# Kernel tuning notes

Hardware: AMD Instinct MI355X
Metric: run time of the kernel (lower is better)

The kernel has to match this reference:

```python
import jax, jax.numpy as jnp
import numpy as np

B, M, K, C = 256, 512, 6, 32  # graphs, nodes/graph, knn k, channels
IN_DIM, OUT_DIM = 4, 6


def setup_inputs() -> dict:
    key = jax.random.key(0)
    ks = jax.random.split(key, 20)
    N = B * M
    x = jax.random.normal(ks[0], (N, 1), dtype=jnp.float32)
    pos = jax.random.uniform(ks[1], (N, 3), dtype=jnp.float32)
    batch = jnp.repeat(jnp.arange(B, dtype=jnp.int64), M)

    def lin(k, out_d, in_d):
        bound = 1.0 / np.sqrt(in_d)
        kw, kb = jax.random.split(k)
        W = jax.random.uniform(kw, (out_d, in_d), minval=-bound, maxval=bound, dtype=jnp.float32)
        b = jax.random.uniform(kb, (out_d,), minval=-bound, maxval=bound, dtype=jnp.float32)
        return W, b

    W1a, b1a = lin(ks[2], C, IN_DIM)
    W2a, b2a = lin(ks[3], C, C)
    W1b, b1b = lin(ks[4], C, C)
    W2b, b2b = lin(ks[5], C, C)
    W1c, b1c = lin(ks[6], C, C)
    W2c, b2c = lin(ks[7], C, C)
    Wr, br = lin(ks[8], OUT_DIM, C)
    return dict(x=x, pos=pos, batch=batch,
                W1a=W1a, b1a=b1a, W2a=W2a, b2a=b2a,
                W1b=W1b, b1b=b1b, W2b=W2b, b2b=b2b,
                W1c=W1c, b1c=b1c, W2c=W2c, b2c=b2c,
                Wr=Wr, br=br)


def knn_indices(pos3):
    # pos3: [B, M, 3] -> [B, M, K] indices of K nearest neighbors (self included, loop=True)
    sq = jnp.sum(pos3 * pos3, axis=-1)                      # [B, M]
    d2 = sq[:, :, None] + sq[:, None, :] - 2.0 * jnp.einsum('bmd,bnd->bmn', pos3, pos3)
    _, idx = jax.lax.top_k(-d2, K)                          # [B, M, K]
    return idx


def gcn_layer(h, idx, W1, b1, W2, b2):
    # h: [B, M, Cin]; gather h_j per edge, 2-layer MLP per edge, max-aggregate over neighbors
    Cin = h.shape[-1]
    nb = jnp.take_along_axis(h, idx.reshape(B, M * K, 1), axis=1).reshape(B, M, K, Cin)
    msg = jax.nn.relu(jnp.einsum('bmkc,oc->bmko', nb, W1) + b1)
    msg = jnp.einsum('bmkc,oc->bmko', msg, W2) + b2
    return jnp.max(msg, axis=2)                             # max aggregation -> [B, M, C]


def reference(x, pos, batch,
              W1a, b1a, W2a, b2a,
              W1b, b1b, W2b, b2b,
              W1c, b1c, W2c, b2c,
              Wr, br):
    pos3 = pos.reshape(B, M, 3)
    idx = knn_indices(pos3)
    h = jnp.concatenate([x, pos], axis=-1).reshape(B, M, IN_DIM)
    h = jax.nn.relu(gcn_layer(h, idx, W1a, b1a, W2a, b2a))
    h = jax.nn.relu(gcn_layer(h, idx, W1b, b1b, W2b, b2b))
    h = jax.nn.relu(gcn_layer(h, idx, W1c, b1c, W2c, b2c))
    g = jnp.max(h, axis=1)                                  # global_max_pool -> [B, C]
    return g @ Wr.T + br                                    # [B, 6]
```

## Files before the change

### kernel.cpp

```cpp
#include <hip/hip_runtime.h>
#include <cstddef>

#define NB 256
#define M 512
#define KNN 6
#define C 32

__global__ __launch_bounds__(1024, 1) void megafused_kernel(
    const float* __restrict__ x, const float* __restrict__ pos,
    const float* __restrict__ W1a, const float* __restrict__ b1a,
    const float* __restrict__ W2a, const float* __restrict__ b2a,
    const float* __restrict__ W1b, const float* __restrict__ b1b,
    const float* __restrict__ W2b, const float* __restrict__ b2b,
    const float* __restrict__ W1c, const float* __restrict__ b1c,
    const float* __restrict__ W2c, const float* __restrict__ b2c,
    const float* __restrict__ Wr,  const float* __restrict__ br,
    float* __restrict__ out)
{
    __shared__ __align__(16) float Ts[M * C];
    const int g  = blockIdx.x;
    const int t  = threadIdx.x;
    const int n  = t & (M - 1);
    const int hv = t >> 9;
    const int c0 = __builtin_amdgcn_readfirstlane(hv << 4);

    float4* sp          = (float4*)Ts;
    float*  cd          = Ts + 2048;
    unsigned short* ci  = (unsigned short*)(Ts + 2048 + 7168);

    const float* p = pos + (size_t)g * M * 3;
    if (t < M) {
        float xx = p[3*t], yy = p[3*t+1], zz = p[3*t+2];
        sp[t] = make_float4(xx, yy, zz, fmaf(xx, xx, fmaf(yy, yy, zz * zz)));
    }
    __syncthreads();

    const float4 pm = sp[n];

    float d0 = INFINITY, d1 = INFINITY, d2 = INFINITY,
          d3 = INFINITY, d4 = INFINITY, d5 = INFINITY;
    int   i0 = -1, i1 = -1, i2 = -1, i3 = -1, i4 = -1, i5 = -1;

    const int col0 = hv << 8;
#pragma unroll 4
    for (int jj = 0; jj < 256; jj++) {
        const int col = col0 + jj;
        const float4 pn = sp[col];
        float dot  = fmaf(pm.x, pn.x, fmaf(pm.y, pn.y, pm.z * pn.z));
        float dist = fmaf(-2.f, dot, pm.w + pn.w);
        bool c5 = dist < d5, c4 = dist < d4, c3 = dist < d3,
             c2 = dist < d2, c1 = dist < d1, cz = dist < d0;
        i5 = c4 ? i4 : (c5 ? col : i5);
        i4 = c3 ? i3 : (c4 ? col : i4);
        i3 = c2 ? i2 : (c3 ? col : i3);
        i2 = c1 ? i1 : (c2 ? col : i2);
        i1 = cz ? i0 : (c1 ? col : i1);
        i0 = cz ? col : i0;
        d5 = __builtin_amdgcn_fmed3f(dist, d4, d5);
        d4 = __builtin_amdgcn_fmed3f(dist, d3, d4);
        d3 = __builtin_amdgcn_fmed3f(dist, d2, d3);
        d2 = __builtin_amdgcn_fmed3f(dist, d1, d2);
        d1 = __builtin_amdgcn_fmed3f(dist, d0, d1);
        d0 = fminf(dist, d0);
    }
    {
        float* cdp = cd + t * 7;
        cdp[0]=d0; cdp[1]=d1; cdp[2]=d2; cdp[3]=d3; cdp[4]=d4; cdp[5]=d5;
        unsigned short* cip = ci + t * 7;
        cip[0]=(unsigned short)i0; cip[1]=(unsigned short)i1;
        cip[2]=(unsigned short)i2; cip[3]=(unsigned short)i3;
        cip[4]=(unsigned short)i4; cip[5]=(unsigned short)i5;
    }
    __syncthreads();

    int j[KNN];
    {
        float md[KNN]; int mi[KNN];
#pragma unroll
        for (int k = 0; k < KNN; k++) { md[k] = cd[n*7 + k]; mi[k] = ci[n*7 + k]; }
        const int L1 = (n + M) * 7;
#pragma unroll
        for (int k = 0; k < KNN; k++) {
            float dist = cd[L1 + k];
            int   nn   = ci[L1 + k];
            bool c5 = dist < md[5], c4 = dist < md[4], c3 = dist < md[3],
                 c2 = dist < md[2], c1 = dist < md[1], cz = dist < md[0];
            mi[5] = c4 ? mi[4] : (c5 ? nn : mi[5]);
            mi[4] = c3 ? mi[3] : (c4 ? nn : mi[4]);
            mi[3] = c2 ? mi[2] : (c3 ? nn : mi[3]);
            mi[2] = c1 ? mi[1] : (c2 ? nn : mi[2]);
            mi[1] = cz ? mi[0] : (c1 ? nn : mi[1]);
            mi[0] = cz ? nn : mi[0];
            md[5] = __builtin_amdgcn_fmed3f(dist, md[4], md[5]);
            md[4] = __builtin_amdgcn_fmed3f(dist, md[3], md[4]);
            md[3] = __builtin_amdgcn_fmed3f(dist, md[2], md[3]);
            md[2] = __builtin_amdgcn_fmed3f(dist, md[1], md[2]);
            md[1] = __builtin_amdgcn_fmed3f(dist, md[0], md[1]);
            md[0] = fminf(dist, md[0]);
        }
#pragma unroll
        for (int k = 0; k < KNN; k++) j[k] = mi[k];
    }
    __syncthreads();

    const int np = n & 7;

    {
        const float h0 = x[(size_t)g * M + n];
        const float h1 = pm.x, h2 = pm.y, h3 = pm.z;
        float m1[C];
#pragma unroll
        for (int o = 0; o < C; o++) {
            float a = b1a[o];
            a = fmaf(W1a[o*4+0], h0, a);
            a = fmaf(W1a[o*4+1], h1, a);
            a = fmaf(W1a[o*4+2], h2, a);
            a = fmaf(W1a[o*4+3], h3, a);
            m1[o] = fmaxf(a, 0.f);
        }
#pragma unroll
        for (int q2 = 0; q2 < 4; q2++) {
            float4 v; float* vp = &v.x;
#pragma unroll
            for (int u = 0; u < 4; u++) {
                const int o = c0 + q2*4 + u;
                float a = b2a[o];
#pragma unroll
                for (int i = 0; i < C; i++) a = fmaf(W2a[o*C + i], m1[i], a);
                vp[u] = a;
            }
            const int q = 4*hv + q2;
            *(float4*)&Ts[n*C + ((q ^ np) << 2)] = v;
        }
    }
    __syncthreads();

#pragma unroll 1
    for (int layer = 0; layer < 2; layer++) {
        const float* W1 = layer ? W1c : W1b;
        const float* b1 = layer ? b1c : b1b;
        const float* W2 = layer ? W2c : W2b;
        const float* b2 = layer ? b2c : b2b;

        float hm[16];
#pragma unroll
        for (int u = 0; u < 16; u++) hm[u] = 0.f;
#pragma unroll
        for (int k = 0; k < KNN; k++) {
            const int jl = j[k], jp = jl & 7;
#pragma unroll
            for (int q2 = 0; q2 < 4; q2++) {
                const int q = 4*hv + q2;
                const float4 v = *(const float4*)&Ts[jl*C + ((q ^ jp) << 2)];
                hm[4*q2+0] = fmaxf(hm[4*q2+0], v.x);
                hm[4*q2+1] = fmaxf(hm[4*q2+1], v.y);
                hm[4*q2+2] = fmaxf(hm[4*q2+2], v.z);
                hm[4*q2+3] = fmaxf(hm[4*q2+3], v.w);
            }
        }
        __syncthreads();
#pragma unroll
        for (int q2 = 0; q2 < 4; q2++) {
            const int q = 4*hv + q2;
            *(float4*)&Ts[n*C + ((q ^ np) << 2)] =
                make_float4(hm[4*q2], hm[4*q2+1], hm[4*q2+2], hm[4*q2+3]);
        }
        __syncthreads();
        float hf[C];
#pragma unroll
        for (int q = 0; q < 8; q++) {
            const float4 v = *(const float4*)&Ts[n*C + ((q ^ np) << 2)];
            hf[4*q+0] = v.x; hf[4*q+1] = v.y; hf[4*q+2] = v.z; hf[4*q+3] = v.w;
        }
        __syncthreads();
        float m1h[16];
#pragma unroll
        for (int o2 = 0; o2 < 16; o2++) {
            const int o = c0 + o2;
            float a = b1[o];
#pragma unroll
            for (int i = 0; i < C; i++) a = fmaf(W1[o*C + i], hf[i], a);
            m1h[o2] = fmaxf(a, 0.f);
        }
#pragma unroll
        for (int q2 = 0; q2 < 4; q2++) {
            const int q = 4*hv + q2;
            *(float4*)&Ts[n*C + ((q ^ np) << 2)] =
                make_float4(m1h[4*q2], m1h[4*q2+1], m1h[4*q2+2], m1h[4*q2+3]);
        }
        __syncthreads();
        float m1[C];
#pragma unroll
        for (int q = 0; q < 8; q++) {
            const float4 v = *(const float4*)&Ts[n*C + ((q ^ np) << 2)];
            m1[4*q+0] = v.x; m1[4*q+1] = v.y; m1[4*q+2] = v.z; m1[4*q+3] = v.w;
        }
        __syncthreads();
#pragma unroll
        for (int q2 = 0; q2 < 4; q2++) {
            float4 v; float* vp = &v.x;
#pragma unroll
            for (int u = 0; u < 4; u++) {
                const int o = c0 + q2*4 + u;
                float a = b2[o];
#pragma unroll
                for (int i = 0; i < C; i++) a = fmaf(W2[o*C + i], m1[i], a);
                vp[u] = a;
            }
            const int q = 4*hv + q2;
            *(float4*)&Ts[n*C + ((q ^ np) << 2)] = v;
        }
        __syncthreads();
    }

    {
        float hm[16];
#pragma unroll
        for (int u = 0; u < 16; u++) hm[u] = 0.f;
#pragma unroll
        for (int k = 0; k < KNN; k++) {
            const int jl = j[k], jp = jl & 7;
#pragma unroll
            for (int q2 = 0; q2 < 4; q2++) {
                const int q = 4*hv + q2;
                const float4 v = *(const float4*)&Ts[jl*C + ((q ^ jp) << 2)];
                hm[4*q2+0] = fmaxf(hm[4*q2+0], v.x);
                hm[4*q2+1] = fmaxf(hm[4*q2+1], v.y);
                hm[4*q2+2] = fmaxf(hm[4*q2+2], v.z);
                hm[4*q2+3] = fmaxf(hm[4*q2+3], v.w);
            }
        }
        __syncthreads();
#pragma unroll
        for (int q2 = 0; q2 < 4; q2++) {
            const int q = 4*hv + q2;
            *(float4*)&Ts[n*C + ((q ^ np) << 2)] =
                make_float4(hm[4*q2], hm[4*q2+1], hm[4*q2+2], hm[4*q2+3]);
        }
        __syncthreads();
    }

    const int tp = t & 7;
    for (int s = 256; s >= 32; s >>= 1) {
        if (t < s) {
#pragma unroll
            for (int q = 0; q < 8; q++) {
                const int ph = (q ^ tp) << 2;
                float4 a = *(const float4*)&Ts[t*C + ph];
                float4 b = *(const float4*)&Ts[(t + s)*C + ph];
                a.x = fmaxf(a.x, b.x); a.y = fmaxf(a.y, b.y);
                a.z = fmaxf(a.z, b.z); a.w = fmaxf(a.w, b.w);
                *(float4*)&Ts[t*C + ph] = a;
            }
        }
        __syncthreads();
    }

    if (t < C) {
        float m = -INFINITY;
#pragma unroll
        for (int r = 0; r < 32; r++)
            m = fmaxf(m, Ts[r*C + ((((t >> 2) ^ (r & 7)) << 2) | (t & 3))]);
        Ts[t] = m;
    }
    __syncthreads();

    if (t < 6) {
        float a = br[t];
#pragma unroll
        for (int i = 0; i < C; i++) a = fmaf(Wr[t*C + i], Ts[i], a);
        out[g * 6 + t] = a;
    }
}

extern "C" void kernel_launch(void* const* d_in, const int* in_sizes, int n_in,
                              void* d_out, int out_size, void* d_ws, size_t ws_size,
                              hipStream_t stream) {
    const float* x   = (const float*)d_in[0];
    const float* pos = (const float*)d_in[1];
    const float* W1a = (const float*)d_in[3];
    const float* b1a = (const float*)d_in[4];
    const float* W2a = (const float*)d_in[5];
    const float* b2a = (const float*)d_in[6];
    const float* W1b = (const float*)d_in[7];
    const float* b1b = (const float*)d_in[8];
    const float* W2b = (const float*)d_in[9];
    const float* b2b = (const float*)d_in[10];
    const float* W1c = (const float*)d_in[11];
    const float* b1c = (const float*)d_in[12];
    const float* W2c = (const float*)d_in[13];
    const float* b2c = (const float*)d_in[14];
    const float* Wr  = (const float*)d_in[15];
    const float* br  = (const float*)d_in[16];

    float* out = (float*)d_out;

    megafused_kernel<<<NB, 1024, 0, stream>>>(x, pos,
                                              W1a, b1a, W2a, b2a,
                                              W1b, b1b, W2b, b2b,
                                              W1c, b1c, W2c, b2c,
                                              Wr, br, out);
}
```

Baseline: 180.1 us.

## Drop final neighbor gather, reuse register halves, pack kNN merge lists

Measured after the change: 172.9 us. 1.04x faster.

```diff
diff --git a/kernel.cpp b/kernel.cpp
--- a/kernel.cpp
+++ b/kernel.cpp
@@ -1,5 +1,6 @@
 #include <hip/hip_runtime.h>
 #include <cstddef>
+#include <cstdint>
 
 #define NB 256
 #define M 512
@@ -24,9 +25,8 @@
     const int hv = t >> 9;
     const int c0 = __builtin_amdgcn_readfirstlane(hv << 4);
 
-    float4* sp          = (float4*)Ts;
-    float*  cd          = Ts + 2048;
-    unsigned short* ci  = (unsigned short*)(Ts + 2048 + 7168);
+    float4* sp    = (float4*)Ts;
+    float4* lists = (float4*)(Ts + 2048);
 
     const float* p = pos + (size_t)g * M * 3;
     if (t < M) {
@@ -42,7 +42,7 @@
     int   i0 = -1, i1 = -1, i2 = -1, i3 = -1, i4 = -1, i5 = -1;
 
     const int col0 = hv << 8;
-#pragma unroll 4
+#pragma unroll 8
     for (int jj = 0; jj < 256; jj++) {
         const int col = col0 + jj;
         const float4 pn = sp[col];
@@ -63,34 +63,47 @@
         d1 = __builtin_amdgcn_fmed3f(dist, d0, d1);
         d0 = fminf(dist, d0);
     }
+
     {
-        float* cdp = cd + t * 7;
-        cdp[0]=d0; cdp[1]=d1; cdp[2]=d2; cdp[3]=d3; cdp[4]=d4; cdp[5]=d5;
-        unsigned short* cip = ci + t * 7;
-        cip[0]=(unsigned short)i0; cip[1]=(unsigned short)i1;
-        cip[2]=(unsigned short)i2; cip[3]=(unsigned short)i3;
-        cip[4]=(unsigned short)i4; cip[5]=(unsigned short)i5;
+        unsigned pa = (unsigned)i0 | ((unsigned)i1 << 10) | ((unsigned)i2 << 20);
+        unsigned pb = (unsigned)i3 | ((unsigned)i4 << 10) | ((unsigned)i5 << 20);
+        lists[2*t]     = make_float4(d0, d1, d2, d3);
+        lists[2*t + 1] = make_float4(d4, d5, __uint_as_float(pa), __uint_as_float(pb));
     }
     __syncthreads();
 
     int j[KNN];
     {
-        float md[KNN]; int mi[KNN];
-#pragma unroll
-        for (int k = 0; k < KNN; k++) { md[k] = cd[n*7 + k]; mi[k] = ci[n*7 + k]; }
-        const int L1 = (n + M) * 7;
+        const int pt = t ^ M;
+        const float4 q0 = lists[2*pt], q1 = lists[2*pt + 1];
+        const unsigned ppa = __float_as_uint(q1.z), ppb = __float_as_uint(q1.w);
+
+        float md[KNN]; int mi[KNN]; float sd[KNN]; int si[KNN];
+        if (c0 == 0) {
+            md[0]=d0; md[1]=d1; md[2]=d2; md[3]=d3; md[4]=d4; md[5]=d5;
+            mi[0]=i0; mi[1]=i1; mi[2]=i2; mi[3]=i3; mi[4]=i4; mi[5]=i5;
+            sd[0]=q0.x; sd[1]=q0.y; sd[2]=q0.z; sd[3]=q0.w; sd[4]=q1.x; sd[5]=q1.y;
+            si[0]=(int)(ppa & 1023); si[1]=(int)((ppa >> 10) & 1023); si[2]=(int)((ppa >> 20) & 1023);
+            si[3]=(int)(ppb & 1023); si[4]=(int)((ppb >> 10) & 1023); si[5]=(int)((ppb >> 20) & 1023);
+        } else {
+            md[0]=q0.x; md[1]=q0.y; md[2]=q0.z; md[3]=q0.w; md[4]=q1.x; md[5]=q1.y;
+            mi[0]=(int)(ppa & 1023); mi[1]=(int)((ppa >> 10) & 1023); mi[2]=(int)((ppa >> 20) & 1023);
+            mi[3]=(int)(ppb & 1023); mi[4]=(int)((ppb >> 10) & 1023); mi[5]=(int)((ppb >> 20) & 1023);
+            sd[0]=d0; sd[1]=d1; sd[2]=d2; sd[3]=d3; sd[4]=d4; sd[5]=d5;
+            si[0]=i0; si[1]=i1; si[2]=i2; si[3]=i3; si[4]=i4; si[5]=i5;
+        }
 #pragma unroll
         for (int k = 0; k < KNN; k++) {
-            float dist = cd[L1 + k];
-            int   nn   = ci[L1 + k];
-            bool c5 = dist < md[5], c4 = dist < md[4], c3 = dist < md[3],
-                 c2 = dist < md[2], c1 = dist < md[1], cz = dist < md[0];
-            mi[5] = c4 ? mi[4] : (c5 ? nn : mi[5]);
-            mi[4] = c3 ? mi[3] : (c4 ? nn : mi[4]);
-            mi[3] = c2 ? mi[2] : (c3 ? nn : mi[3]);
-            mi[2] = c1 ? mi[1] : (c2 ? nn : mi[2]);
-            mi[1] = cz ? mi[0] : (c1 ? nn : mi[1]);
-            mi[0] = cz ? nn : mi[0];
+            const float dist = sd[k];
+            const int   nn   = si[k];
+            bool c5m = dist < md[5], c4m = dist < md[4], c3m = dist < md[3],
+                 c2m = dist < md[2], c1m = dist < md[1], czm = dist < md[0];
+            mi[5] = c4m ? mi[4] : (c5m ? nn : mi[5]);
+            mi[4] = c3m ? mi[3] : (c4m ? nn : mi[4]);
+            mi[3] = c2m ? mi[2] : (c3m ? nn : mi[3]);
+            mi[2] = c1m ? mi[1] : (c2m ? nn : mi[2]);
+            mi[1] = czm ? mi[0] : (c1m ? nn : mi[1]);
+            mi[0] = czm ? nn : mi[0];
             md[5] = __builtin_amdgcn_fmed3f(dist, md[4], md[5]);
             md[4] = __builtin_amdgcn_fmed3f(dist, md[3], md[4]);
             md[3] = __builtin_amdgcn_fmed3f(dist, md[2], md[3]);
@@ -103,7 +116,18 @@
     }
     __syncthreads();
 
-    const int np = n & 7;
+    const int ne     = n & 3;
+    const int nb_own = (n << 7) + ((hv ^ ((n >> 2) & 1)) << 6);
+    const int nb_par = nb_own ^ 64;
+    char* TsB = (char*)Ts;
+
+    int jb[KNN], je[KNN];
+#pragma unroll
+    for (int k = 0; k < KNN; k++) {
+        const int jl = j[k];
+        jb[k] = (jl << 7) + ((hv ^ ((jl >> 2) & 1)) << 6);
+        je[k] = jl & 3;
+    }
 
     {
         const float h0 = x[(size_t)g * M + n];
@@ -129,8 +153,7 @@
                 for (int i = 0; i < C; i++) a = fmaf(W2a[o*C + i], m1[i], a);
                 vp[u] = a;
             }
-            const int q = 4*hv + q2;
-            *(float4*)&Ts[n*C + ((q ^ np) << 2)] = v;
+            *(float4*)(TsB + nb_own + ((q2 ^ ne) << 4)) = v;
         }
     }
     __syncthreads();
@@ -147,11 +170,9 @@
         for (int u = 0; u < 16; u++) hm[u] = 0.f;
 #pragma unroll
         for (int k = 0; k < KNN; k++) {
-            const int jl = j[k], jp = jl & 7;
-#pragma unroll
-            for (int q2 = 0; q2 < 4; q2++) {
-                const int q = 4*hv + q2;
-                const float4 v = *(const float4*)&Ts[jl*C + ((q ^ jp) << 2)];
+#pragma unroll
+            for (int q2 = 0; q2 < 4; q2++) {
+                const float4 v = *(const float4*)(TsB + jb[k] + ((q2 ^ je[k]) << 4));
                 hm[4*q2+0] = fmaxf(hm[4*q2+0], v.x);
                 hm[4*q2+1] = fmaxf(hm[4*q2+1], v.y);
                 hm[4*q2+2] = fmaxf(hm[4*q2+2], v.z);
@@ -160,17 +181,27 @@
         }
         __syncthreads();
 #pragma unroll
-        for (int q2 = 0; q2 < 4; q2++) {
-            const int q = 4*hv + q2;
-            *(float4*)&Ts[n*C + ((q ^ np) << 2)] =
-                make_float4(hm[4*q2], hm[4*q2+1], hm[4*q2+2], hm[4*q2+3]);
-        }
+        for (int q2 = 0; q2 < 4; q2++)
+            *(float4*)(TsB + nb_own + ((q2 ^ ne) << 4)) =
+                make_float4(hm[4*q2+0], hm[4*q2+1], hm[4*q2+2], hm[4*q2+3]);
         __syncthreads();
         float hf[C];
-#pragma unroll
-        for (int q = 0; q < 8; q++) {
-            const float4 v = *(const float4*)&Ts[n*C + ((q ^ np) << 2)];
-            hf[4*q+0] = v.x; hf[4*q+1] = v.y; hf[4*q+2] = v.z; hf[4*q+3] = v.w;
+        if (c0 == 0) {
+#pragma unroll
+            for (int u = 0; u < 16; u++) hf[u] = hm[u];
+#pragma unroll
+            for (int q2 = 0; q2 < 4; q2++) {
+                const float4 v = *(const float4*)(TsB + nb_par + ((q2 ^ ne) << 4));
+                hf[16+4*q2+0]=v.x; hf[16+4*q2+1]=v.y; hf[16+4*q2+2]=v.z; hf[16+4*q2+3]=v.w;
+            }
+        } else {
+#pragma unroll
+            for (int u = 0; u < 16; u++) hf[16+u] = hm[u];
+#pragma unroll
+            for (int q2 = 0; q2 < 4; q2++) {
+                const float4 v = *(const float4*)(TsB + nb_par + ((q2 ^ ne) << 4));
+                hf[4*q2+0]=v.x; hf[4*q2+1]=v.y; hf[4*q2+2]=v.z; hf[4*q2+3]=v.w;
+            }
         }
         __syncthreads();
         float m1h[16];
@@ -183,17 +214,27 @@
             m1h[o2] = fmaxf(a, 0.f);
         }
 #pragma unroll
-        for (int q2 = 0; q2 < 4; q2++) {
-            const int q = 4*hv + q2;
-            *(float4*)&Ts[n*C + ((q ^ np) << 2)] =
-                make_float4(m1h[4*q2], m1h[4*q2+1], m1h[4*q2+2], m1h[4*q2+3]);
-        }
-        __syncthreads();
-        float m1[C];
-#pragma unroll
-        for (int q = 0; q < 8; q++) {
-            const float4 v = *(const float4*)&Ts[n*C + ((q ^ np) << 2)];
-            m1[4*q+0] = v.x; m1[4*q+1] = v.y; m1[4*q+2] = v.z; m1[4*q+3] = v.w;
+        for (int q2 = 0; q2 < 4; q2++)
+            *(float4*)(TsB + nb_own + ((q2 ^ ne) << 4)) =
+                make_float4(m1h[4*q2+0], m1h[4*q2+1], m1h[4*q2+2], m1h[4*q2+3]);
+        __syncthreads();
+        float m1f[C];
+        if (c0 == 0) {
+#pragma unroll
+            for (int u = 0; u < 16; u++) m1f[u] = m1h[u];
+#pragma unroll
+            for (int q2 = 0; q2 < 4; q2++) {
+                const float4 v = *(const float4*)(TsB + nb_par + ((q2 ^ ne) << 4));
+                m1f[16+4*q2+0]=v.x; m1f[16+4*q2+1]=v.y; m1f[16+4*q2+2]=v.z; m1f[16+4*q2+3]=v.w;
+            }
+        } else {
+#pragma unroll
+            for (int u = 0; u < 16; u++) m1f[16+u] = m1h[u];
+#pragma unroll
+            for (int q2 = 0; q2 < 4; q2++) {
+                const float4 v = *(const float4*)(TsB + nb_par + ((q2 ^ ne) << 4));
+                m1f[4*q2+0]=v.x; m1f[4*q2+1]=v.y; m1f[4*q2+2]=v.z; m1f[4*q2+3]=v.w;
+            }
         }
         __syncthreads();
 #pragma unroll
@@ -204,66 +245,35 @@
                 const int o = c0 + q2*4 + u;
                 float a = b2[o];
 #pragma unroll
-                for (int i = 0; i < C; i++) a = fmaf(W2[o*C + i], m1[i], a);
+                for (int i = 0; i < C; i++) a = fmaf(W2[o*C + i], m1f[i], a);
                 vp[u] = a;
             }
-            const int q = 4*hv + q2;
-            *(float4*)&Ts[n*C + ((q ^ np) << 2)] = v;
+            *(float4*)(TsB + nb_own + ((q2 ^ ne) << 4)) = v;
         }
         __syncthreads();
     }
 
     {
-        float hm[16];
-#pragma unroll
-        for (int u = 0; u < 16; u++) hm[u] = 0.f;
-#pragma unroll
-        for (int k = 0; k < KNN; k++) {
-            const int jl = j[k], jp = jl & 7;
-#pragma unroll
-            for (int q2 = 0; q2 < 4; q2++) {
-                const int q = 4*hv + q2;
-                const float4 v = *(const float4*)&Ts[jl*C + ((q ^ jp) << 2)];
-                hm[4*q2+0] = fmaxf(hm[4*q2+0], v.x);
-                hm[4*q2+1] = fmaxf(hm[4*q2+1], v.y);
-                hm[4*q2+2] = fmaxf(hm[4*q2+2], v.z);
-                hm[4*q2+3] = fmaxf(hm[4*q2+3], v.w);
-            }
-        }
-        __syncthreads();
-#pragma unroll
-        for (int q2 = 0; q2 < 4; q2++) {
-            const int q = 4*hv + q2;
-            *(float4*)&Ts[n*C + ((q ^ np) << 2)] =
-                make_float4(hm[4*q2], hm[4*q2+1], hm[4*q2+2], hm[4*q2+3]);
-        }
-        __syncthreads();
-    }
-
-    const int tp = t & 7;
-    for (int s = 256; s >= 32; s >>= 1) {
-        if (t < s) {
-#pragma unroll
-            for (int q = 0; q < 8; q++) {
-                const int ph = (q ^ tp) << 2;
-                float4 a = *(const float4*)&Ts[t*C + ph];
-                float4 b = *(const float4*)&Ts[(t + s)*C + ph];
-                a.x = fmaxf(a.x, b.x); a.y = fmaxf(a.y, b.y);
-                a.z = fmaxf(a.z, b.z); a.w = fmaxf(a.w, b.w);
-                *(float4*)&Ts[t*C + ph] = a;
-            }
-        }
-        __syncthreads();
-    }
-
-    if (t < C) {
-        float m = -INFINITY;
-#pragma unroll
-        for (int r = 0; r < 32; r++)
-            m = fmaxf(m, Ts[r*C + ((((t >> 2) ^ (r & 7)) << 2) | (t & 3))]);
-        Ts[t] = m;
-    }
-    __syncthreads();
+        const int c   = t & 31;
+        const int grp = t >> 5;
+        float m = 0.f;
+#pragma unroll
+        for (int r16 = 0; r16 < 16; r16++) {
+            const int r = (grp << 4) + r16;
+            m = fmaxf(m, Ts[(r << 5) + ((((c >> 2) ^ (r & 7)) << 2) | (c & 3))]);
+        }
+        __syncthreads();
+        Ts[(grp << 5) + (c ^ grp)] = m;
+        __syncthreads();
+        if (t < 32) {
+            float mm = 0.f;
+#pragma unroll
+            for (int g2 = 0; g2 < 32; g2++)
+                mm = fmaxf(mm, Ts[(g2 << 5) + (t ^ g2)]);
+            Ts[t] = mm;
+        }
+        __syncthreads();
+    }
 
     if (t < 6) {
         float a = br[t];
```
